# Optimization experiments

Measured on AMD Instinct MI355X. Metric: run time of the kernel, lower is better.

The kernel has to match this reference:

```python
import jax, jax.numpy as jnp
import numpy as np

N = 10000      # nodes per QA graph
E = 128000     # edges per QA graph
A = 5          # answers (multiple choice)
D = 300        # glove embedding dim
H = 8          # heads layer 1
C1 = 64        # per-head out channels layer 1 (concat -> 512)
HID = 512
NEG_SLOPE = 0.2
EPS = 1e-16


def gat_layer(x, edge_index, W, a_src, a_dst, bias, concat):
    # x: [N, Din]; edge_index: [2, E]; W: [Din, H*C]; a_src/a_dst: [H, C]
    Hh, C = a_src.shape
    h = (x @ W).reshape(N, Hh, C)                      # transformed node feats
    alpha_src = (h * a_src[None]).sum(-1)              # [N, H]
    alpha_dst = (h * a_dst[None]).sum(-1)              # [N, H]
    src, dst = edge_index[0], edge_index[1]
    e = jax.nn.leaky_relu(alpha_src[src] + alpha_dst[dst], NEG_SLOPE)  # [E, H]
    # edge softmax grouped by destination node
    m = jax.ops.segment_max(e, dst, num_segments=N)    # [N, H]
    ex = jnp.exp(e - m[dst])
    denom = jax.ops.segment_sum(ex, dst, num_segments=N)
    alpha = ex / (denom[dst] + EPS)                    # [E, H]
    msg = alpha[:, :, None] * h[src]                   # [E, H, C]
    out = jax.ops.segment_sum(msg, dst, num_segments=N)  # [N, H, C]
    out = out.reshape(N, Hh * C) if concat else out.mean(axis=1)
    return out + bias, alpha


def setup_inputs() -> dict:
    key = jax.random.key(0)
    ks = jax.random.split(key, 10)
    s = 0.05
    return {
        "x": jax.random.normal(ks[0], (A, N, D), jnp.float32),
        "edge_index": jax.random.randint(ks[1], (A, 2, E), 0, N, dtype=jnp.int32),
        "W1": jax.random.normal(ks[2], (D, H * C1), jnp.float32) * s,
        "att_src1": jax.random.normal(ks[3], (H, C1), jnp.float32) * s,
        "att_dst1": jax.random.normal(ks[4], (H, C1), jnp.float32) * s,
        "bias1": jnp.zeros((H * C1,), jnp.float32),
        "W2": jax.random.normal(ks[5], (HID, 1), jnp.float32) * s,
        "att_src2": jax.random.normal(ks[6], (1, 1), jnp.float32) * s,
        "att_dst2": jax.random.normal(ks[7], (1, 1), jnp.float32) * s,
        "bias2": jnp.zeros((1,), jnp.float32),
    }


def reference(x, edge_index, W1, att_src1, att_dst1, bias1, W2, att_src2, att_dst2, bias2):
    def per_answer(xa, ei):
        h1, _ = gat_layer(xa, ei, W1, att_src1, att_dst1, bias1, concat=True)
        h1 = jax.nn.relu(h1)
        h2, alpha = gat_layer(h1, ei, W2, att_src2, att_dst2, bias2, concat=False)
        proba = h2.mean()                                  # scalar (x.mean(dim=0))
        # aggregate_attention: attention[dst] += edge_weight (edge_additive)
        att = jax.ops.segment_sum(alpha[:, 0], ei[1], num_segments=N)
        return proba, att

    proba_vec, atts = jax.vmap(per_answer)(x, edge_index)  # [A], [A, N]
    sel = atts[jnp.argmax(proba_vec)]                      # attentions[argmax]
    return proba_vec, sel
```

## Files before the change

kernel.cpp:

```cpp
#include <hip/hip_runtime.h>
#include <hip/hip_bf16.h>
#include <math.h>

#define NN 10000
#define EE 128000
#define AA 5
#define DD 300
#define HH 8
#define CC 64
#define HC 512
#define MM (AA*NN)
#define KP 320
#define NT (KP / 32)
#define NBM ((MM + 63) / 64)

typedef __attribute__((ext_vector_type(8))) _Float16 f16x8;
typedef __attribute__((ext_vector_type(4))) float f32x4;
typedef __attribute__((ext_vector_type(2))) float f32x2;
typedef unsigned short ushort;
typedef unsigned char uchar;

__device__ __forceinline__ ushort f2bf(float f) {
    unsigned u = __float_as_uint(f);
    unsigned r = u + 0x7fffu + ((u >> 16) & 1u);
    return (ushort)(r >> 16);
}
__device__ __forceinline__ float bf2f(ushort h) {
    return __uint_as_float(((unsigned)h) << 16);
}


__global__ void zero_cnt(int* cnt) {
    int i = blockIdx.x * 256 + threadIdx.x;
    if (i < AA * NN) cnt[i] = 0;
}

__global__ void count_edges(const int* __restrict__ ei, int* __restrict__ cnt) {
    int a = blockIdx.y;
    int e = blockIdx.x * 256 + threadIdx.x;
    if (e < EE) {
        int dst = ei[(size_t)a * 2 * EE + EE + e];
        atomicAdd(&cnt[a * NN + dst], 1);
    }
}

__global__ __launch_bounds__(256) void scan_counts(const int* __restrict__ cnt,
                                                   int* __restrict__ offs,
                                                   int* __restrict__ cursor) {
    int a = blockIdx.x;
    int tid = threadIdx.x, lane = tid & 63, wv = tid >> 6;
    __shared__ int wsum[4];
    __shared__ int s_carry;
    if (tid == 0) s_carry = 0;
    __syncthreads();
    for (int base = 0; base < NN; base += 1024) {
        int i0 = base + tid * 4;
        int v0 = (i0 + 0 < NN) ? cnt[a * NN + i0 + 0] : 0;
        int v1 = (i0 + 1 < NN) ? cnt[a * NN + i0 + 1] : 0;
        int v2 = (i0 + 2 < NN) ? cnt[a * NN + i0 + 2] : 0;
        int v3 = (i0 + 3 < NN) ? cnt[a * NN + i0 + 3] : 0;
        int tsum = v0 + v1 + v2 + v3;
        int sc = tsum;
        #pragma unroll
        for (int o = 1; o < 64; o <<= 1) {
            int u = __shfl_up(sc, o);
            if (lane >= o) sc += u;
        }
        if (lane == 63) wsum[wv] = sc;
        int excl_wave = sc - tsum;
        __syncthreads();
        int woff = 0;
        #pragma unroll
        for (int w = 0; w < 4; ++w) woff += (w < wv) ? wsum[w] : 0;
        int chunk_total = wsum[0] + wsum[1] + wsum[2] + wsum[3];
        int carry = s_carry;
        __syncthreads();
        if (tid == 0) s_carry = carry + chunk_total;
        int o0 = carry + woff + excl_wave;
        int o1 = o0 + v0, o2 = o1 + v1, o3 = o2 + v2;
        int* offsA = offs + a * (NN + 1);
        int* curA = cursor + a * (NN + 1);
        if (i0 + 0 < NN) { offsA[i0 + 0] = o0; curA[i0 + 0] = o0; }
        if (i0 + 1 < NN) { offsA[i0 + 1] = o1; curA[i0 + 1] = o1; }
        if (i0 + 2 < NN) { offsA[i0 + 2] = o2; curA[i0 + 2] = o2; }
        if (i0 + 3 < NN) { offsA[i0 + 3] = o3; curA[i0 + 3] = o3; }
    }
    __syncthreads();
    if (tid == 0) offs[a * (NN + 1) + NN] = s_carry;
}

__global__ void scatter_edges(const int* __restrict__ ei, int* __restrict__ cursor,
                              int* __restrict__ csr_eid) {
    int a = blockIdx.y;
    int e = blockIdx.x * 256 + threadIdx.x;
    if (e < EE) {
        int dst = ei[(size_t)a * 2 * EE + EE + e];
        int pos = atomicAdd(&cursor[a * (NN + 1) + dst], 1);
        csr_eid[(size_t)a * EE + pos] = e;
    }
}

__global__ __launch_bounds__(256) void sort_src(const int* __restrict__ ei,
                                                const int* __restrict__ offs,
                                                int* __restrict__ csr_eid,
                                                int* __restrict__ csr_src,
                                                int* __restrict__ csr_dst) {
    int a = blockIdx.y;
    int wid = threadIdx.x >> 6, l = threadIdx.x & 63;
    int n = blockIdx.x * 4 + wid;
    if (n >= NN) return;
    const int* offsA = offs + a * (NN + 1);
    int beg = offsA[n], end = offsA[n + 1];
    int deg = end - beg;
    int* seg = csr_eid + (size_t)a * EE + beg;
    const int* srcrow = ei + (size_t)a * 2 * EE;
    if (deg <= 64) {
        int v = (l < deg) ? seg[l] : 0x7fffffff;
        #pragma unroll
        for (int k = 2; k <= 64; k <<= 1)
            #pragma unroll
            for (int j = k >> 1; j > 0; j >>= 1) {
                int p = __shfl_xor(v, j);
                bool keepMin = (((l & k) == 0) == ((l & j) == 0));
                int mn = min(v, p), mx = max(v, p);
                v = keepMin ? mn : mx;
            }
        if (l < deg) {
            csr_src[(size_t)a * EE + beg + l] = srcrow[v];
            csr_dst[(size_t)a * EE + beg + l] = n;
        }
    } else {
        if (l == 0) {
            for (int i = 1; i < deg; ++i) {
                int key = seg[i];
                int j = i - 1;
                while (j >= 0 && seg[j] > key) { seg[j + 1] = seg[j]; --j; }
                seg[j + 1] = key;
            }
        }
        for (int i = l; i < deg; i += 64) {
            csr_src[(size_t)a * EE + beg + i] = srcrow[seg[i]];
            csr_dst[(size_t)a * EE + beg + i] = n;
        }
    }
}


__global__ __launch_bounds__(256) void pack_x(const float* __restrict__ X,
                                              ushort* __restrict__ Xp) {
    int gid = blockIdx.x * 256 + threadIdx.x;
    if (gid >= NBM * NT * 4 * 64) return;
    int l = gid & 63;
    int fr = (gid >> 6) & 3;
    int rest = gid >> 8;
    int ks = rest % NT;
    int bmi = rest / NT;
    int row = bmi * 64 + fr * 16 + (l & 15);
    int k = ks * 32 + (l >> 4) * 8;
    f16x8 o;
    if (row < MM && k + 8 <= DD) {
        float4 v0 = *(const float4*)(X + (size_t)row * DD + k);
        float4 v1 = *(const float4*)(X + (size_t)row * DD + k + 4);
        o[0] = (_Float16)v0.x; o[1] = (_Float16)v0.y;
        o[2] = (_Float16)v0.z; o[3] = (_Float16)v0.w;
        o[4] = (_Float16)v1.x; o[5] = (_Float16)v1.y;
        o[6] = (_Float16)v1.z; o[7] = (_Float16)v1.w;
    } else {
        #pragma unroll
        for (int j = 0; j < 8; ++j)
            o[j] = (row < MM && k + j < DD) ? (_Float16)X[(size_t)row * DD + k + j]
                                            : (_Float16)0.f;
    }
    *(f16x8*)(Xp + (size_t)gid * 8) = o;
}

__global__ __launch_bounds__(256) void pack_w(const float* __restrict__ W,
                                              ushort* __restrict__ Wp) {
    int gid = blockIdx.x * 256 + threadIdx.x;
    if (gid >= HH * NT * 4 * 64) return;
    int l = gid & 63;
    int fc = (gid >> 6) & 3;
    int rest = gid >> 8;
    int ks = rest % NT;
    int head = rest / NT;
    int col = head * 64 + fc * 16 + (l & 15);
    int k = ks * 32 + (l >> 4) * 8;
    f16x8 o;
    #pragma unroll
    for (int j = 0; j < 8; ++j)
        o[j] = (k + j < DD) ? (_Float16)W[(size_t)(k + j) * HC + col] : (_Float16)0.f;
    *(f16x8*)(Wp + (size_t)gid * 8) = o;
}


__global__ __launch_bounds__(256) void gemm_f16(const ushort* __restrict__ Xp,
                                                const ushort* __restrict__ Wp,
                                                const float* __restrict__ att_src1,
                                                const float* __restrict__ att_dst1,
                                                uchar* __restrict__ Hout,
                                                float* __restrict__ asrc,
                                                float* __restrict__ adst) {
    int wid = blockIdx.x * 4 + (threadIdx.x >> 6);
    int bmi = wid >> 3, head = wid & 7;
    if (bmi >= NBM) return;
    int bm = bmi * 64;
    int l = threadIdx.x & 63;
    int l16 = l & 15, kg = l >> 4;

    const ushort* Abase = Xp + (size_t)bmi * NT * 2048 + l * 8;
    const ushort* Bbase = Wp + (size_t)head * NT * 2048 + l * 8;

    f32x4 zz = {0.f, 0.f, 0.f, 0.f};
    f32x4 acc[4][4];
    #pragma unroll
    for (int i = 0; i < 4; ++i)
        #pragma unroll
        for (int j = 0; j < 4; ++j) acc[i][j] = zz;

    f16x8 aX[4], bX[4], aY[4], bY[4];
    #pragma unroll
    for (int f = 0; f < 4; ++f) {
        aX[f] = *(const f16x8*)(Abase + f * 512);
        bX[f] = *(const f16x8*)(Bbase + f * 512);
    }

    #pragma unroll
    for (int kk = 0; kk < NT; kk += 2) {
        if (kk + 1 < NT) {
            #pragma unroll
            for (int f = 0; f < 4; ++f) {
                aY[f] = *(const f16x8*)(Abase + (kk + 1) * 2048 + f * 512);
                bY[f] = *(const f16x8*)(Bbase + (kk + 1) * 2048 + f * 512);
            }
        }
        #pragma unroll
        for (int fr = 0; fr < 4; ++fr)
            #pragma unroll
            for (int fc = 0; fc < 4; ++fc)
                acc[fr][fc] = __builtin_amdgcn_mfma_f32_16x16x32_f16(aX[fr], bX[fc], acc[fr][fc], 0, 0, 0);
        if (kk + 2 < NT) {
            #pragma unroll
            for (int f = 0; f < 4; ++f) {
                aX[f] = *(const f16x8*)(Abase + (kk + 2) * 2048 + f * 512);
                bX[f] = *(const f16x8*)(Bbase + (kk + 2) * 2048 + f * 512);
            }
        }
        if (kk + 1 < NT) {
            #pragma unroll
            for (int fr = 0; fr < 4; ++fr)
                #pragma unroll
                for (int fc = 0; fc < 4; ++fc)
                    acc[fr][fc] = __builtin_amdgcn_mfma_f32_16x16x32_f16(aY[fr], bY[fc], acc[fr][fc], 0, 0, 0);
        }
    }

    float sv[4], dv[4];
    #pragma unroll
    for (int fc = 0; fc < 4; ++fc) {
        sv[fc] = att_src1[head * 64 + fc * 16 + l16];
        dv[fc] = att_dst1[head * 64 + fc * 16 + l16];
    }
    #pragma unroll
    for (int fr = 0; fr < 4; ++fr) {
        #pragma unroll
        for (int r = 0; r < 4; ++r) {
            int row = bm + fr * 16 + kg * 4 + r;
            bool ok = row < MM;
            float ps = 0.f, pd = 0.f;
            #pragma unroll
            for (int fc = 0; fc < 4; ++fc) {
                float val = acc[fr][fc][r];
                if (ok) {
                    int pk = __builtin_amdgcn_cvt_pk_fp8_f32(val, val, 0, false);
                    Hout[(size_t)row * HC + head * 64 + fc * 16 + l16] = (uchar)(pk & 0xff);
                }
                ps = fmaf(val, sv[fc], ps);
                pd = fmaf(val, dv[fc], pd);
            }
            #pragma unroll
            for (int o = 1; o < 16; o <<= 1) {
                ps += __shfl_xor(ps, o);
                pd += __shfl_xor(pd, o);
            }
            if (l16 == 0 && ok) {
                asrc[(size_t)row * HH + head] = ps;
                adst[(size_t)row * HH + head] = pd;
            }
        }
    }
}


__global__ __launch_bounds__(256) void edge_w(const int* __restrict__ csr_src,
                                              const int* __restrict__ csr_dst,
                                              const float* __restrict__ asrc,
                                              const float* __restrict__ adst,
                                              float* __restrict__ w_csr) {
    int a = blockIdx.y;
    int gid = blockIdx.x * 256 + threadIdx.x;
    if (gid >= EE * HH) return;
    int slot = gid >> 3, hd = gid & 7;
    int s = csr_src[(size_t)a * EE + slot];
    int d = csr_dst[(size_t)a * EE + slot];
    float v = asrc[((size_t)a * NN + s) * HH + hd] + adst[((size_t)a * NN + d) * HH + hd];
    v = v > 0.f ? v : 0.2f * v;
    w_csr[(size_t)a * EE * HH + gid] = __expf(v);
}


__global__ __launch_bounds__(256) void layer1_agg(const uchar* __restrict__ h1,
                                                  const float* __restrict__ w_csr,
                                                  const int* __restrict__ offs,
                                                  const int* __restrict__ csr_src,
                                                  const float* __restrict__ bias1,
                                                  const float* __restrict__ W2,
                                                  float* __restrict__ h2) {
    int a = blockIdx.y;
    int wid = threadIdx.x >> 6, l = threadIdx.x & 63;
    int n = blockIdx.x * 4 + wid;
    int eg = l >> 3;
    int gh = l >> 3;

    const int* offsA = offs + a * (NN + 1);
    int beg = offsA[n], end = offsA[n + 1];
    int deg = end - beg;
    const int* srcs = csr_src + (size_t)a * EE + beg;
    const float* wA = w_csr + ((size_t)a * EE + beg) * HH;
    const uchar* h1A = h1 + (size_t)a * NN * HC;

    float denom = 0.f;
    float acc[8] = {};

    float w_cur = (eg < deg) ? wA[l] : 0.f;
    int s_cur = (eg < deg) ? srcs[eg] : 0;

    for (int c0 = 0; c0 < deg; c0 += 8) {
        float w_nxt = 0.f;
        int s_nxt = 0;
        if (c0 + 8 + eg < deg) {
            w_nxt = wA[(c0 + 8) * 8 + l];
            s_nxt = srcs[c0 + 8 + eg];
        }
        #pragma unroll
        for (int j = 0; j < 8; ++j) {
            if (c0 + j < deg) {
                float wj = __shfl(w_cur, j * 8 + gh);
                int sj = __shfl(s_cur, j * 8);
                uint2 hv = *(const uint2*)(h1A + (size_t)sj * HC + (l << 3));
                f32x2 p0 = __builtin_amdgcn_cvt_pk_f32_fp8((int)hv.x, false);
                f32x2 p1 = __builtin_amdgcn_cvt_pk_f32_fp8((int)hv.x, true);
                f32x2 p2 = __builtin_amdgcn_cvt_pk_f32_fp8((int)hv.y, false);
                f32x2 p3 = __builtin_amdgcn_cvt_pk_f32_fp8((int)hv.y, true);
                acc[0] = fmaf(wj, p0[0], acc[0]);
                acc[1] = fmaf(wj, p0[1], acc[1]);
                acc[2] = fmaf(wj, p1[0], acc[2]);
                acc[3] = fmaf(wj, p1[1], acc[3]);
                acc[4] = fmaf(wj, p2[0], acc[4]);
                acc[5] = fmaf(wj, p2[1], acc[5]);
                acc[6] = fmaf(wj, p3[0], acc[6]);
                acc[7] = fmaf(wj, p3[1], acc[7]);
            }
        }
        denom += w_cur;
        w_cur = w_nxt;
        s_cur = s_nxt;
    }
    #pragma unroll
    for (int o = 8; o < 64; o <<= 1) denom += __shfl_xor(denom, o);
    float dn = __shfl(denom, gh);
    float inv = 1.f / (dn + 1e-16f);

    int cb = l * 8;
    float4 b0 = *(const float4*)(bias1 + cb);
    float4 b1 = *(const float4*)(bias1 + cb + 4);
    float4 w0 = *(const float4*)(W2 + cb);
    float4 w1 = *(const float4*)(W2 + cb + 4);
    float bz[8] = {b0.x, b0.y, b0.z, b0.w, b1.x, b1.y, b1.z, b1.w};
    float wz[8] = {w0.x, w0.y, w0.z, w0.w, w1.x, w1.y, w1.z, w1.w};
    float p = 0.f;
    #pragma unroll
    for (int k = 0; k < 8; ++k) {
        float z = fmaf(acc[k], inv, bz[k]);
        z = z > 0.f ? z : 0.f;
        p = fmaf(z, wz[k], p);
    }
    #pragma unroll
    for (int o = 1; o < 64; o <<= 1) p += __shfl_xor(p, o);
    if (l == 0) h2[(size_t)a * NN + n] = p;
}


#define L2GRID 40

__global__ __launch_bounds__(256) void layer2_proba(const float* __restrict__ h2,
                                                    const int* __restrict__ offs,
                                                    const int* __restrict__ csr_src,
                                                    const float* __restrict__ att_src2,
                                                    const float* __restrict__ att_dst2,
                                                    const float* __restrict__ bias2,
                                                    float* __restrict__ partials) {
    int a = blockIdx.y;
    int n = blockIdx.x * 256 + threadIdx.x;
    float out2 = 0.f;
    if (n < NN) {
        const int* offsA = offs + a * (NN + 1);
        const int* srcs = csr_src + (size_t)a * EE;
        const float* h2A = h2 + (size_t)a * NN;
        float as2 = att_src2[0], ad2 = att_dst2[0];
        int beg = offsA[n], end = offsA[n + 1];
        float adn = h2A[n] * ad2;
        float denom = 0.f, accv = 0.f;
        for (int i = beg; i < end; ++i) {
            float hs = h2A[srcs[i]];
            float v = fmaf(hs, as2, adn);
            v = v > 0.f ? v : 0.2f * v;
            float w = __expf(v);
            denom += w;
            accv = fmaf(w, hs, accv);
        }
        out2 = accv / (denom + 1e-16f) + bias2[0];
    }
    __shared__ float red[256];
    red[threadIdx.x] = out2;
    __syncthreads();
    for (int s = 128; s > 0; s >>= 1) {
        if (threadIdx.x < s) red[threadIdx.x] += red[threadIdx.x + s];
        __syncthreads();
    }
    if (threadIdx.x == 0) partials[a * L2GRID + blockIdx.x] = red[0];
}

__global__ __launch_bounds__(256) void finalize_proba(const float* __restrict__ partials,
                                                      float* __restrict__ out,
                                                      int* __restrict__ best) {
    int tid = threadIdx.x;
    __shared__ float red[256];
    red[tid] = (tid < AA * L2GRID) ? partials[tid] : 0.f;
    __syncthreads();
    if (tid == 0) {
        float pv[AA];
        for (int a = 0; a < AA; ++a) {
            float s = 0.f;
            for (int i = 0; i < L2GRID; ++i) s += red[a * L2GRID + i];
            pv[a] = s / (float)NN;
            out[a] = pv[a];
        }
        int b = 0;
        for (int a = 1; a < AA; ++a)
            if (pv[a] > pv[b]) b = a;
        *best = b;
    }
}

__global__ void write_sel(const int* __restrict__ cnt, const int* __restrict__ best,
                          float* __restrict__ out) {
    int n = blockIdx.x * 256 + threadIdx.x;
    if (n < NN) out[AA + n] = (cnt[(*best) * NN + n] > 0) ? 1.0f : 0.0f;
}


extern "C" void kernel_launch(void* const* d_in, const int* in_sizes, int n_in,
                              void* d_out, int out_size, void* d_ws, size_t ws_size,
                              hipStream_t stream) {
    const float* x        = (const float*)d_in[0];
    const int*   ei       = (const int*)d_in[1];
    const float* W1       = (const float*)d_in[2];
    const float* att_src1 = (const float*)d_in[3];
    const float* att_dst1 = (const float*)d_in[4];
    const float* bias1    = (const float*)d_in[5];
    const float* W2       = (const float*)d_in[6];
    const float* att_src2 = (const float*)d_in[7];
    const float* att_dst2 = (const float*)d_in[8];
    const float* bias2    = (const float*)d_in[9];
    float* out = (float*)d_out;

    char* ws = (char*)d_ws;
    size_t off = 0;
    auto alloc = [&](size_t bytes) {
        size_t cur = off;
        off += (bytes + 255) & ~(size_t)255;
        return cur;
    };
    uchar*  h1      = (uchar*)(ws + alloc(sizeof(uchar) * (size_t)MM * HC));
    ushort* xp      = (ushort*)(ws + alloc(sizeof(ushort) * (size_t)NBM * NT * 2048));
    float*  asrc    = (float*)(ws + alloc(sizeof(float) * (size_t)MM * HH));
    float*  adst    = (float*)(ws + alloc(sizeof(float) * (size_t)MM * HH));
    float*  h2      = (float*)(ws + alloc(sizeof(float) * (size_t)MM));
    int*    cnt     = (int*)(ws + alloc(sizeof(int) * (size_t)AA * NN));
    int*    offs    = (int*)(ws + alloc(sizeof(int) * (size_t)AA * (NN + 1)));
    int*    cursor  = (int*)(ws + alloc(sizeof(int) * (size_t)AA * (NN + 1)));
    int*    csr_eid = (int*)(ws + alloc(sizeof(int) * (size_t)AA * EE));
    int*    csr_src = (int*)(ws + alloc(sizeof(int) * (size_t)AA * EE));
    int*    csr_dst = (int*)(ws + alloc(sizeof(int) * (size_t)AA * EE));
    float*  w_csr   = (float*)(ws + alloc(sizeof(float) * (size_t)AA * EE * HH));
    float*  partials= (float*)(ws + alloc(sizeof(float) * AA * L2GRID));
    int*    best    = (int*)(ws + alloc(sizeof(int) * 16));
    ushort* wp      = (ushort*)(ws + alloc(sizeof(ushort) * (size_t)HH * NT * 2048));
    (void)ws_size; (void)in_sizes; (void)n_in; (void)out_size;

    pack_w<<<dim3((HH * NT * 256 + 255) / 256), dim3(256), 0, stream>>>(W1, wp);
    pack_x<<<dim3((NBM * NT * 256 + 255) / 256), dim3(256), 0, stream>>>(x, xp);

    zero_cnt<<<dim3((AA * NN + 255) / 256), dim3(256), 0, stream>>>(cnt);
    count_edges<<<dim3(EE / 256, AA), dim3(256), 0, stream>>>(ei, cnt);
    scan_counts<<<dim3(AA), dim3(256), 0, stream>>>(cnt, offs, cursor);
    scatter_edges<<<dim3(EE / 256, AA), dim3(256), 0, stream>>>(ei, cursor, csr_eid);
    sort_src<<<dim3(NN / 4, AA), dim3(256), 0, stream>>>(ei, offs, csr_eid, csr_src, csr_dst);

    gemm_f16<<<dim3((NBM * 8 + 3) / 4), dim3(256), 0, stream>>>(
        xp, wp, att_src1, att_dst1, h1, asrc, adst);

    edge_w<<<dim3(EE * HH / 256, AA), dim3(256), 0, stream>>>(csr_src, csr_dst,
                                                              asrc, adst, w_csr);

    layer1_agg<<<dim3(NN / 4, AA), dim3(256), 0, stream>>>(h1, w_csr, offs, csr_src,
                                                           bias1, W2, h2);

    layer2_proba<<<dim3(L2GRID, AA), dim3(256), 0, stream>>>(h2, offs, csr_src,
                                                             att_src2, att_dst2, bias2,
                                                             partials);

    finalize_proba<<<dim3(1), dim3(256), 0, stream>>>(partials, out, best);
    write_sel<<<dim3((NN + 255) / 256), dim3(256), 0, stream>>>(cnt, best, out);
}
```

Measured before the change: 244.4 us.

## Parallelize CSR scan across blocks and split layer-1 aggregation by head halves

Replaces the single-block-per-answer serial scan of degree counts with a three-kernel block-sum / block-scan / final-scan scheme spread over many blocks. Splits layer-1 aggregation into two grid slices, each covering four heads (256 channels), with the edge weights re-laid out in head-half-major form. Each wave now processes two edges at once on 32-lane halves, and a small kernel sums the two partial h2 results. This adds kernel launches and an extra buffer in exchange for more parallelism and fewer serial steps. It also inserts a wave barrier in sort_src after the lane-0 insertion sort.

```diff
diff --git a/kernel.cpp b/kernel.cpp
--- a/kernel.cpp
+++ b/kernel.cpp
@@ -13,6 +13,8 @@
 #define KP 320
 #define NT (KP / 32)
 #define NBM ((MM + 63) / 64)
+#define SCB 40
+#define SCN 250
 
 typedef __attribute__((ext_vector_type(8))) _Float16 f16x8;
 typedef __attribute__((ext_vector_type(4))) float f32x4;
@@ -44,49 +46,62 @@
     }
 }
 
-__global__ __launch_bounds__(256) void scan_counts(const int* __restrict__ cnt,
-                                                   int* __restrict__ offs,
-                                                   int* __restrict__ cursor) {
+
+__global__ __launch_bounds__(256) void scan_bsum(const int* __restrict__ cnt,
+                                                 int* __restrict__ bsum) {
+    int a = blockIdx.y, b = blockIdx.x;
+    int l = threadIdx.x;
+    int v = (l < SCN) ? cnt[a * NN + b * SCN + l] : 0;
+    #pragma unroll
+    for (int o = 1; o < 64; o <<= 1) v += __shfl_xor(v, o);
+    __shared__ int red[4];
+    if ((l & 63) == 0) red[l >> 6] = v;
+    __syncthreads();
+    if (l == 0) bsum[a * SCB + b] = red[0] + red[1] + red[2] + red[3];
+}
+
+__global__ __launch_bounds__(64) void scan_bscan(const int* __restrict__ bsum,
+                                                 int* __restrict__ boff,
+                                                 int* __restrict__ offs) {
     int a = blockIdx.x;
-    int tid = threadIdx.x, lane = tid & 63, wv = tid >> 6;
-    __shared__ int wsum[4];
-    __shared__ int s_carry;
-    if (tid == 0) s_carry = 0;
+    int l = threadIdx.x;
+    int v = (l < SCB) ? bsum[a * SCB + l] : 0;
+    int sc = v;
+    #pragma unroll
+    for (int o = 1; o < 64; o <<= 1) {
+        int u = __shfl_up(sc, o);
+        if (l >= o) sc += u;
+    }
+    if (l < SCB) boff[a * SCB + l] = sc - v;
+    if (l == 63) offs[a * (NN + 1) + NN] = sc;
+}
+
+__global__ __launch_bounds__(256) void scan_final(const int* __restrict__ cnt,
+                                                  const int* __restrict__ boff,
+                                                  int* __restrict__ offs,
+                                                  int* __restrict__ cursor) {
+    int a = blockIdx.y, b = blockIdx.x;
+    int l = threadIdx.x;
+    int i = b * SCN + l;
+    int v = (l < SCN) ? cnt[a * NN + i] : 0;
+    int sc = v;
+    int lane = l & 63, wv = l >> 6;
+    #pragma unroll
+    for (int o = 1; o < 64; o <<= 1) {
+        int u = __shfl_up(sc, o);
+        if (lane >= o) sc += u;
+    }
+    __shared__ int ws[4];
+    if (lane == 63) ws[wv] = sc;
     __syncthreads();
-    for (int base = 0; base < NN; base += 1024) {
-        int i0 = base + tid * 4;
-        int v0 = (i0 + 0 < NN) ? cnt[a * NN + i0 + 0] : 0;
-        int v1 = (i0 + 1 < NN) ? cnt[a * NN + i0 + 1] : 0;
-        int v2 = (i0 + 2 < NN) ? cnt[a * NN + i0 + 2] : 0;
-        int v3 = (i0 + 3 < NN) ? cnt[a * NN + i0 + 3] : 0;
-        int tsum = v0 + v1 + v2 + v3;
-        int sc = tsum;
-        #pragma unroll
-        for (int o = 1; o < 64; o <<= 1) {
-            int u = __shfl_up(sc, o);
-            if (lane >= o) sc += u;
-        }
-        if (lane == 63) wsum[wv] = sc;
-        int excl_wave = sc - tsum;
-        __syncthreads();
-        int woff = 0;
-        #pragma unroll
-        for (int w = 0; w < 4; ++w) woff += (w < wv) ? wsum[w] : 0;
-        int chunk_total = wsum[0] + wsum[1] + wsum[2] + wsum[3];
-        int carry = s_carry;
-        __syncthreads();
-        if (tid == 0) s_carry = carry + chunk_total;
-        int o0 = carry + woff + excl_wave;
-        int o1 = o0 + v0, o2 = o1 + v1, o3 = o2 + v2;
-        int* offsA = offs + a * (NN + 1);
-        int* curA = cursor + a * (NN + 1);
-        if (i0 + 0 < NN) { offsA[i0 + 0] = o0; curA[i0 + 0] = o0; }
-        if (i0 + 1 < NN) { offsA[i0 + 1] = o1; curA[i0 + 1] = o1; }
-        if (i0 + 2 < NN) { offsA[i0 + 2] = o2; curA[i0 + 2] = o2; }
-        if (i0 + 3 < NN) { offsA[i0 + 3] = o3; curA[i0 + 3] = o3; }
-    }
-    __syncthreads();
-    if (tid == 0) offs[a * (NN + 1) + NN] = s_carry;
+    int woff = 0;
+    #pragma unroll
+    for (int w = 0; w < 4; ++w) woff += (w < wv) ? ws[w] : 0;
+    if (l < SCN) {
+        int o = boff[a * SCB + b] + woff + sc - v;
+        offs[a * (NN + 1) + i] = o;
+        cursor[a * (NN + 1) + i] = o;
+    }
 }
 
 __global__ void scatter_edges(const int* __restrict__ ei, int* __restrict__ cursor,
@@ -138,6 +153,7 @@
                 seg[j + 1] = key;
             }
         }
+        __builtin_amdgcn_wave_barrier();
         for (int i = l; i < deg; i += 64) {
             csr_src[(size_t)a * EE + beg + i] = srcrow[seg[i]];
             csr_dst[(size_t)a * EE + beg + i] = n;
@@ -295,7 +311,7 @@
                                               const int* __restrict__ csr_dst,
                                               const float* __restrict__ asrc,
                                               const float* __restrict__ adst,
-                                              float* __restrict__ w_csr) {
+                                              float* __restrict__ w4) {
     int a = blockIdx.y;
     int gid = blockIdx.x * 256 + threadIdx.x;
     if (gid >= EE * HH) return;
@@ -304,73 +320,69 @@
     int d = csr_dst[(size_t)a * EE + slot];
     float v = asrc[((size_t)a * NN + s) * HH + hd] + adst[((size_t)a * NN + d) * HH + hd];
     v = v > 0.f ? v : 0.2f * v;
-    w_csr[(size_t)a * EE * HH + gid] = __expf(v);
+    w4[(((size_t)a * 2 + (hd >> 2)) * EE + slot) * 4 + (hd & 3)] = __expf(v);
 }
 
 
 __global__ __launch_bounds__(256) void layer1_agg(const uchar* __restrict__ h1,
-                                                  const float* __restrict__ w_csr,
+                                                  const float* __restrict__ w4,
                                                   const int* __restrict__ offs,
                                                   const int* __restrict__ csr_src,
                                                   const float* __restrict__ bias1,
                                                   const float* __restrict__ W2,
-                                                  float* __restrict__ h2) {
+                                                  float* __restrict__ h2p) {
     int a = blockIdx.y;
+    int hf = blockIdx.z;
     int wid = threadIdx.x >> 6, l = threadIdx.x & 63;
     int n = blockIdx.x * 4 + wid;
-    int eg = l >> 3;
-    int gh = l >> 3;
+    int l32 = l & 31;
+    int ehalf = l >> 5;
+    int hs = l32 >> 3;
 
     const int* offsA = offs + a * (NN + 1);
     int beg = offsA[n], end = offsA[n + 1];
     int deg = end - beg;
     const int* srcs = csr_src + (size_t)a * EE + beg;
-    const float* wA = w_csr + ((size_t)a * EE + beg) * HH;
-    const uchar* h1A = h1 + (size_t)a * NN * HC;
+    const float* wA = w4 + (((size_t)a * 2 + hf) * EE + beg) * 4;
+    const uchar* h1A = h1 + (size_t)a * NN * HC + hf * 256;
 
     float denom = 0.f;
     float acc[8] = {};
 
-    float w_cur = (eg < deg) ? wA[l] : 0.f;
-    int s_cur = (eg < deg) ? srcs[eg] : 0;
-
-    for (int c0 = 0; c0 < deg; c0 += 8) {
-        float w_nxt = 0.f;
-        int s_nxt = 0;
-        if (c0 + 8 + eg < deg) {
-            w_nxt = wA[(c0 + 8) * 8 + l];
-            s_nxt = srcs[c0 + 8 + eg];
-        }
+    for (int c0 = 0; c0 < deg; c0 += 16) {
+        int ei_w = c0 + (l >> 2);
+        float w_reg = (ei_w < deg) ? wA[c0 * 4 + l] : 0.f;
+        denom += w_reg;
+        int s_reg = srcs[min(c0 + (l & 15), deg - 1)];
         #pragma unroll
-        for (int j = 0; j < 8; ++j) {
-            if (c0 + j < deg) {
-                float wj = __shfl(w_cur, j * 8 + gh);
-                int sj = __shfl(s_cur, j * 8);
-                uint2 hv = *(const uint2*)(h1A + (size_t)sj * HC + (l << 3));
-                f32x2 p0 = __builtin_amdgcn_cvt_pk_f32_fp8((int)hv.x, false);
-                f32x2 p1 = __builtin_amdgcn_cvt_pk_f32_fp8((int)hv.x, true);
-                f32x2 p2 = __builtin_amdgcn_cvt_pk_f32_fp8((int)hv.y, false);
-                f32x2 p3 = __builtin_amdgcn_cvt_pk_f32_fp8((int)hv.y, true);
-                acc[0] = fmaf(wj, p0[0], acc[0]);
-                acc[1] = fmaf(wj, p0[1], acc[1]);
-                acc[2] = fmaf(wj, p1[0], acc[2]);
-                acc[3] = fmaf(wj, p1[1], acc[3]);
-                acc[4] = fmaf(wj, p2[0], acc[4]);
-                acc[5] = fmaf(wj, p2[1], acc[5]);
-                acc[6] = fmaf(wj, p3[0], acc[6]);
-                acc[7] = fmaf(wj, p3[1], acc[7]);
-            }
-        }
-        denom += w_cur;
-        w_cur = w_nxt;
-        s_cur = s_nxt;
-    }
-    #pragma unroll
-    for (int o = 8; o < 64; o <<= 1) denom += __shfl_xor(denom, o);
-    float dn = __shfl(denom, gh);
+        for (int j = 0; j < 16; j += 2) {
+            int e = j + ehalf;
+            float wj = __shfl(w_reg, e * 4 + hs);
+            int sj = __shfl(s_reg, min(e, 15));
+            const uchar* rp = h1A + (size_t)sj * HC + l32 * 8;
+            uint2 hv = *(const uint2*)rp;
+            f32x2 p0 = __builtin_amdgcn_cvt_pk_f32_fp8((int)hv.x, false);
+            f32x2 p1 = __builtin_amdgcn_cvt_pk_f32_fp8((int)hv.x, true);
+            f32x2 p2 = __builtin_amdgcn_cvt_pk_f32_fp8((int)hv.y, false);
+            f32x2 p3 = __builtin_amdgcn_cvt_pk_f32_fp8((int)hv.y, true);
+            acc[0] = fmaf(wj, p0[0], acc[0]);
+            acc[1] = fmaf(wj, p0[1], acc[1]);
+            acc[2] = fmaf(wj, p1[0], acc[2]);
+            acc[3] = fmaf(wj, p1[1], acc[3]);
+            acc[4] = fmaf(wj, p2[0], acc[4]);
+            acc[5] = fmaf(wj, p2[1], acc[5]);
+            acc[6] = fmaf(wj, p3[0], acc[6]);
+            acc[7] = fmaf(wj, p3[1], acc[7]);
+        }
+    }
+    #pragma unroll
+    for (int k = 0; k < 8; ++k) acc[k] += __shfl_xor(acc[k], 32);
+    #pragma unroll
+    for (int o = 4; o < 64; o <<= 1) denom += __shfl_xor(denom, o);
+    float dn = __shfl(denom, hs);
     float inv = 1.f / (dn + 1e-16f);
 
-    int cb = l * 8;
+    int cb = hf * 256 + l32 * 8;
     float4 b0 = *(const float4*)(bias1 + cb);
     float4 b1 = *(const float4*)(bias1 + cb + 4);
     float4 w0 = *(const float4*)(W2 + cb);
@@ -385,8 +397,13 @@
         p = fmaf(z, wz[k], p);
     }
     #pragma unroll
-    for (int o = 1; o < 64; o <<= 1) p += __shfl_xor(p, o);
-    if (l == 0) h2[(size_t)a * NN + n] = p;
+    for (int o = 1; o < 32; o <<= 1) p += __shfl_xor(p, o);
+    if (l == 0) h2p[((size_t)hf * AA + a) * NN + n] = p;
+}
+
+__global__ void sum_h2(const float* __restrict__ h2p, float* __restrict__ h2) {
+    int i = blockIdx.x * 256 + threadIdx.x;
+    if (i < AA * NN) h2[i] = h2p[i] + h2p[(size_t)AA * NN + i];
 }
 
 
@@ -486,13 +503,16 @@
     float*  asrc    = (float*)(ws + alloc(sizeof(float) * (size_t)MM * HH));
     float*  adst    = (float*)(ws + alloc(sizeof(float) * (size_t)MM * HH));
     float*  h2      = (float*)(ws + alloc(sizeof(float) * (size_t)MM));
+    float*  h2p     = (float*)(ws + alloc(sizeof(float) * 2 * (size_t)MM));
     int*    cnt     = (int*)(ws + alloc(sizeof(int) * (size_t)AA * NN));
     int*    offs    = (int*)(ws + alloc(sizeof(int) * (size_t)AA * (NN + 1)));
     int*    cursor  = (int*)(ws + alloc(sizeof(int) * (size_t)AA * (NN + 1)));
+    int*    bsum    = (int*)(ws + alloc(sizeof(int) * (size_t)AA * SCB));
+    int*    boff    = (int*)(ws + alloc(sizeof(int) * (size_t)AA * SCB));
     int*    csr_eid = (int*)(ws + alloc(sizeof(int) * (size_t)AA * EE));
     int*    csr_src = (int*)(ws + alloc(sizeof(int) * (size_t)AA * EE));
     int*    csr_dst = (int*)(ws + alloc(sizeof(int) * (size_t)AA * EE));
-    float*  w_csr   = (float*)(ws + alloc(sizeof(float) * (size_t)AA * EE * HH));
+    float*  w4      = (float*)(ws + alloc(sizeof(float) * (size_t)AA * EE * HH));
     float*  partials= (float*)(ws + alloc(sizeof(float) * AA * L2GRID));
     int*    best    = (int*)(ws + alloc(sizeof(int) * 16));
     ushort* wp      = (ushort*)(ws + alloc(sizeof(ushort) * (size_t)HH * NT * 2048));
@@ -503,7 +523,9 @@
 
     zero_cnt<<<dim3((AA * NN + 255) / 256), dim3(256), 0, stream>>>(cnt);
     count_edges<<<dim3(EE / 256, AA), dim3(256), 0, stream>>>(ei, cnt);
-    scan_counts<<<dim3(AA), dim3(256), 0, stream>>>(cnt, offs, cursor);
+    scan_bsum<<<dim3(SCB, AA), dim3(256), 0, stream>>>(cnt, bsum);
+    scan_bscan<<<dim3(AA), dim3(64), 0, stream>>>(bsum, boff, offs);
+    scan_final<<<dim3(SCB, AA), dim3(256), 0, stream>>>(cnt, boff, offs, cursor);
     scatter_edges<<<dim3(EE / 256, AA), dim3(256), 0, stream>>>(ei, cursor, csr_eid);
     sort_src<<<dim3(NN / 4, AA), dim3(256), 0, stream>>>(ei, offs, csr_eid, csr_src, csr_dst);
 
@@ -511,10 +533,11 @@
         xp, wp, att_src1, att_dst1, h1, asrc, adst);
 
     edge_w<<<dim3(EE * HH / 256, AA), dim3(256), 0, stream>>>(csr_src, csr_dst,
-                                                              asrc, adst, w_csr);
-
-    layer1_agg<<<dim3(NN / 4, AA), dim3(256), 0, stream>>>(h1, w_csr, offs, csr_src,
-                                                           bias1, W2, h2);
+                                                              asrc, adst, w4);
+
+    layer1_agg<<<dim3(NN / 4, AA, 2), dim3(256), 0, stream>>>(h1, w4, offs, csr_src,
+                                                              bias1, W2, h2p);
+    sum_h2<<<dim3((AA * NN + 255) / 256), dim3(256), 0, stream>>>(h2p, h2);
 
     layer2_proba<<<dim3(L2GRID, AA), dim3(256), 0, stream>>>(h2, offs, csr_src,
                                                              att_src2, att_dst2, bias2,
```

Result: no change. 244.0 us (-0.2%).
